# Optimization experiments

Hardware: AMD Instinct MI355X
Metric: run time of the kernel (lower is better)

## Reference

```python
import jax, jax.numpy as jnp
import numpy as np

N_P, N_A, D, H, E = 200000, 100000, 64, 32, 1000000


def setup_inputs() -> dict:
    key = jax.random.key(0)
    ks = jax.random.split(key, 32)
    inp = {}
    inp["x_paper"] = jax.random.normal(ks[0], (N_P, D), jnp.float32)
    inp["x_author"] = jax.random.normal(ks[1], (N_A, D), jnp.float32)
    inp["cites_src"] = jax.random.randint(ks[2], (E,), 0, N_P, jnp.int32)
    inp["cites_dst"] = jax.random.randint(ks[3], (E,), 0, N_P, jnp.int32)
    inp["writes_src"] = jax.random.randint(ks[4], (E,), 0, N_A, jnp.int32)
    inp["writes_dst"] = jax.random.randint(ks[5], (E,), 0, N_P, jnp.int32)
    inp["rev_src"] = jax.random.randint(ks[6], (E,), 0, N_P, jnp.int32)
    inp["rev_dst"] = jax.random.randint(ks[7], (E,), 0, N_A, jnp.int32)
    # per-relation SAGEConv params; layer 1: D->H, layer 2: H->H
    i = 8
    for layer, din in ((1, D), (2, H)):
        for rel in ("cites", "writes", "rev"):
            inp[f"W{layer}l_{rel}"] = 0.1 * jax.random.normal(ks[i], (din, H), jnp.float32); i += 1
            inp[f"W{layer}r_{rel}"] = 0.1 * jax.random.normal(ks[i], (din, H), jnp.float32); i += 1
            inp[f"b{layer}_{rel}"] = 0.01 * jax.random.normal(ks[i], (H,), jnp.float32); i += 1
    return inp


def _sage(x_src, x_dst, src, dst, Wl, Wr, b, n_dst):
    # PyG SAGEConv (aggr='mean'): lin_l(mean of source msgs) + lin_r(x_dst) + bias
    msg = x_src[src]                                              # [E, d] gather
    s = jax.ops.segment_sum(msg, dst, num_segments=n_dst)         # [n_dst, d]
    cnt = jax.ops.segment_sum(jnp.ones((src.shape[0],), x_src.dtype), dst, num_segments=n_dst)
    mean = s / jnp.maximum(cnt, 1.0)[:, None]
    return mean @ Wl + x_dst @ Wr + b


def reference(x_paper, x_author, cites_src, cites_dst, writes_src, writes_dst,
              rev_src, rev_dst,
              W1l_cites, W1r_cites, b1_cites, W1l_writes, W1r_writes, b1_writes,
              W1l_rev, W1r_rev, b1_rev,
              W2l_cites, W2r_cites, b2_cites, W2l_writes, W2r_writes, b2_writes,
              W2l_rev, W2r_rev, b2_rev):
    n_p, n_a = x_paper.shape[0], x_author.shape[0]
    # layer 1 (to_hetero sums relation outputs per dst node type), then relu
    p1 = jax.nn.relu(
        _sage(x_paper, x_paper, cites_src, cites_dst, W1l_cites, W1r_cites, b1_cites, n_p)
        + _sage(x_author, x_paper, writes_src, writes_dst, W1l_writes, W1r_writes, b1_writes, n_p))
    a1 = jax.nn.relu(
        _sage(x_paper, x_author, rev_src, rev_dst, W1l_rev, W1r_rev, b1_rev, n_a))
    # layer 2, return 'paper' output (no activation)
    p2 = (_sage(p1, p1, cites_src, cites_dst, W2l_cites, W2r_cites, b2_cites, n_p)
          + _sage(a1, p1, writes_src, writes_dst, W2l_writes, W2r_writes, b2_writes, n_p))
    return p2
```

## Files before the change

### kernel.cpp

```cpp
#include <hip/hip_runtime.h>

typedef unsigned short u16;
typedef unsigned int   u32;
typedef __attribute__((ext_vector_type(8))) short bf16x8;
typedef __attribute__((ext_vector_type(4))) float f32x4;

#define N_P 200000
#define N_A 100000
#define DD  64
#define HH  32
#define NE  1000000
#define NBP 782
#define NBA 391
#define NB4K 245
#define NCB 196
#define P4CAP 8192
#define NB_P16 12500
#define NB_A16 6250

__device__ inline float bf2f(u16 u) { return __uint_as_float(((u32)u) << 16); }
__device__ inline u16 f2bf(float f) {
    u32 u = __float_as_uint(f);
    u += 0x7fffu + ((u >> 16) & 1u);
    return (u16)(u >> 16);
}
__device__ inline float lo_f(u32 m) { return __uint_as_float(m << 16); }
__device__ inline float hi_f(u32 m) { return __uint_as_float(m & 0xffff0000u); }

__device__ inline void gseg_dual(
    const u16* __restrict__ yA, const int* __restrict__ bkA, int s0, int e0,
    const u16* __restrict__ yB, const int* __restrict__ bkB, int s1, int e1,
    int lane, float& axo, float& ayo, float& bxo, float& byo) {
    float ax = 0.f, ay = 0.f, bx = 0.f, by = 0.f;
    int lastA = min(max(e0 - 1, s0), NE - 1);
    int lastB = min(max(e1 - 1, s1), NE - 1);
    for (int j0 = s0, j1 = s1; (j0 < e0) || (j1 < e1); j0 += 8, j1 += 8) {
        int ia[8], ib[8];
#pragma unroll
        for (int i = 0; i < 8; ++i) ia[i] = bkA[min(j0 + i, lastA)];
#pragma unroll
        for (int i = 0; i < 8; ++i) ib[i] = bkB[min(j1 + i, lastB)];
        u32 ma[8], mb[8];
#pragma unroll
        for (int i = 0; i < 8; ++i)
            ma[i] = *(const u32*)(yA + (size_t)(u32)ia[i] + lane * 2);
#pragma unroll
        for (int i = 0; i < 8; ++i)
            mb[i] = *(const u32*)(yB + (size_t)(u32)ib[i] + lane * 2);
#pragma unroll
        for (int i = 0; i < 8; ++i) {
            u32 va = (j0 + i < e0) ? ma[i] : 0u;
            ax += lo_f(va); ay += hi_f(va);
        }
#pragma unroll
        for (int i = 0; i < 8; ++i) {
            u32 vb = (j1 + i < e1) ? mb[i] : 0u;
            bx += lo_f(vb); by += hi_f(vb);
        }
    }
    axo = ax; ayo = ay; bxo = bx; byo = by;
}

__global__ __launch_bounds__(256) void p1_hist_k(
    const int* __restrict__ cd, const int* __restrict__ wd, const int* __restrict__ rd,
    int* __restrict__ gsizes) {
    int rel = blockIdx.y;
    const int* dst; int shift;
    if (rel == 0)      { dst = cd; shift = 10; }
    else if (rel == 1) { dst = wd; shift = 10; }
    else               { dst = rd; shift = 9;  }
    __shared__ int cnt[256];
    int t = threadIdx.x;
    cnt[t] = 0;
    __syncthreads();
    int e0 = blockIdx.x * 4096;
#pragma unroll
    for (int i = 0; i < 16; ++i) {
        int e = e0 + i * 256 + t;
        if (e < NE) atomicAdd(&cnt[dst[e] >> shift], 1);
    }
    __syncthreads();
    if (t < NCB && cnt[t]) atomicAdd(&gsizes[rel * NCB + t], cnt[t]);
}

__global__ __launch_bounds__(256) void p2_scan_k(
    const int* __restrict__ gsizes, int* __restrict__ bases, int* __restrict__ gcur) {
    __shared__ int lds[256];
    int t = threadIdx.x;
    for (int rel = 0; rel < 3; ++rel) {
        int v = (t < NCB) ? gsizes[rel * NCB + t] : 0;
        lds[t] = v; __syncthreads();
#pragma unroll
        for (int o = 1; o < 256; o <<= 1) {
            int x = (t >= o) ? lds[t - o] : 0;
            __syncthreads();
            lds[t] += x;
            __syncthreads();
        }
        int ex = lds[t] - v;
        if (t < NCB) { bases[rel * NCB + t] = ex; gcur[rel * NCB + t] = ex; }
        __syncthreads();
    }
}

__global__ __launch_bounds__(256) void p3_bin_k(
    const int* __restrict__ cs, const int* __restrict__ cd,
    const int* __restrict__ ws_, const int* __restrict__ wd,
    const int* __restrict__ rs, const int* __restrict__ rd,
    int* __restrict__ gcur,
    u32* __restrict__ pr_c, u32* __restrict__ pr_w, u32* __restrict__ pr_r) {
    int rel = blockIdx.y;
    const int *src, *dst; int shift; u32* out;
    if (rel == 0)      { src = cs;  dst = cd; shift = 10; out = pr_c; }
    else if (rel == 1) { src = ws_; dst = wd; shift = 10; out = pr_w; }
    else               { src = rs;  dst = rd; shift = 9;  out = pr_r; }
    __shared__ u32 sbuf[4096];
    __shared__ int cnt[256], sc[256], lcur[256], gbase[256];
    int t = threadIdx.x;
    cnt[t] = 0;
    __syncthreads();
    int e0 = blockIdx.x * 4096;
    int myd[16];
#pragma unroll
    for (int i = 0; i < 16; ++i) {
        int e = e0 + i * 256 + t;
        myd[i] = (e < NE) ? dst[e] : -1;
        if (myd[i] >= 0) atomicAdd(&cnt[myd[i] >> shift], 1);
    }
    __syncthreads();
    int v = cnt[t];
    sc[t] = v; __syncthreads();
#pragma unroll
    for (int o = 1; o < 256; o <<= 1) {
        int x = (t >= o) ? sc[t - o] : 0;
        __syncthreads();
        sc[t] += x;
        __syncthreads();
    }
    int ex = sc[t] - v;
    __syncthreads();
    sc[t] = ex;
    lcur[t] = ex;
    if (t < NCB) gbase[t] = atomicAdd(&gcur[rel * NCB + t], cnt[t]);
    __syncthreads();
#pragma unroll
    for (int i = 0; i < 16; ++i) {
        int e = e0 + i * 256 + t;
        if (myd[i] >= 0) {
            int d = myd[i];
            int cb = d >> shift;
            u32 dloc = (u32)(d - (cb << shift));
            u32 pk = (dloc << 18) | (u32)src[e];
            int p = atomicAdd(&lcur[cb], 1);
            sbuf[p] = pk;
        }
    }
    __syncthreads();
    int nvalid = min(4096, NE - e0);
    for (int i = t; i < nvalid; i += 256) {
        int lo = 0, hi = NCB - 1;
        while (lo < hi) {
            int mid = (lo + hi + 1) >> 1;
            if (sc[mid] <= i) lo = mid; else hi = mid - 1;
        }
        out[gbase[lo] + (i - sc[lo])] = sbuf[i];
    }
}

__global__ __launch_bounds__(256) void p4_sort_k(
    const int* __restrict__ bases, const int* __restrict__ gsizes,
    const u32* __restrict__ pr_c, const u32* __restrict__ pr_w, const u32* __restrict__ pr_r,
    int* __restrict__ bkt_c, int* __restrict__ bkt_w, int* __restrict__ bkt_r,
    int* __restrict__ st_c, int* __restrict__ st_w, int* __restrict__ st_r) {
    int rel = blockIdx.y;
    const u32* pr; int* bkt; int* st; int width, n;
    if (rel == 0)      { pr = pr_c; bkt = bkt_c; st = st_c; width = 1024; n = N_P; }
    else if (rel == 1) { pr = pr_w; bkt = bkt_w; st = st_w; width = 1024; n = N_P; }
    else               { pr = pr_r; bkt = bkt_r; st = st_r; width = 512;  n = N_A; }
    __shared__ u32 sin[P4CAP];
    __shared__ int cnt[1024], sc2[1024], tmp[256];
    int t = threadIdx.x;
    int b = blockIdx.x;
    int base = bases[rel * NCB + b];
    int size = min(gsizes[rel * NCB + b], P4CAP);
    int d0 = b * width;
    int nd = min(width, n - d0);
    if (nd <= 0) return;
#pragma unroll
    for (int j = t; j < 1024; j += 256) cnt[j] = 0;
    __syncthreads();
    for (int i = t; i < size; i += 256) {
        u32 pk = pr[base + i];
        sin[i] = pk;
        atomicAdd(&cnt[pk >> 18], 1);
    }
    __syncthreads();
    int j0 = 4 * t;
    int c0 = cnt[j0], c1 = cnt[j0 + 1], c2 = cnt[j0 + 2], c3 = cnt[j0 + 3];
    int tot = c0 + c1 + c2 + c3;
    tmp[t] = tot; __syncthreads();
#pragma unroll
    for (int o = 1; o < 256; o <<= 1) {
        int x = (t >= o) ? tmp[t - o] : 0;
        __syncthreads();
        tmp[t] += x;
        __syncthreads();
    }
    int pre = tmp[t] - tot;
    sc2[j0] = pre;
    sc2[j0 + 1] = pre + c0;
    sc2[j0 + 2] = pre + c0 + c1;
    sc2[j0 + 3] = pre + c0 + c1 + c2;
    __syncthreads();
    for (int j = t; j < nd; j += 256) st[d0 + j] = base + sc2[j];
#pragma unroll
    for (int j = t; j < 1024; j += 256) cnt[j] = 0;
    __syncthreads();
    for (int i = t; i < size; i += 256) {
        u32 pk = sin[i];
        int dl = (int)(pk >> 18);
        int pos = sc2[dl] + atomicAdd(&cnt[dl], 1);
        bkt[base + pos] = (int)((pk & 0x3FFFFu) * HH);
    }
}

__global__ __launch_bounds__(256) void prep_w_k(
    const float* __restrict__ W1lc, const float* __restrict__ W1lr,
    const float* __restrict__ W1rc, const float* __restrict__ W1rw,
    const float* __restrict__ W1lw, const float* __restrict__ W1rr,
    const float* __restrict__ W2lc, const float* __restrict__ W2rc,
    const float* __restrict__ W2rw, const float* __restrict__ W2lw,
    const float* __restrict__ b1c, const float* __restrict__ b1w,
    const float* __restrict__ b2c, const float* __restrict__ b2w,
    u16* __restrict__ wt1h, u16* __restrict__ wt1l,
    u16* __restrict__ wt2h, u16* __restrict__ wt2l,
    float* __restrict__ b1s, float* __restrict__ b2s) {
    int m = blockIdx.x, t = threadIdx.x;
    if (m < 5) {
        const float *A = nullptr, *B = nullptr;
        if (m == 0) A = W1lc;
        else if (m == 1) A = W1lr;
        else if (m == 2) { A = W1rc; B = W1rw; }
        else if (m == 3) A = W1lw;
        else A = W1rr;
        for (int e = t; e < 2048; e += 256) {
            int k = e >> 5, n = e & 31;
            float v = A[e] + (B ? B[e] : 0.f);
            u16 h = f2bf(v);
            u16 lw = f2bf(v - bf2f(h));
            wt1h[m * 2048 + n * 64 + k] = h;
            wt1l[m * 2048 + n * 64 + k] = lw;
        }
        if (m == 2 && t < HH) b1s[t] = b1c[t] + b1w[t];
    } else {
        int mm = m - 5;
        const float *A = nullptr, *B = nullptr;
        if (mm == 0) A = W2lc;
        else if (mm == 1) { A = W2rc; B = W2rw; }
        else A = W2lw;
        for (int e = t; e < 1024; e += 256) {
            int k = e >> 5, n = e & 31;
            float v = A[e] + (B ? B[e] : 0.f);
            u16 h = f2bf(v);
            u16 lw = f2bf(v - bf2f(h));
            wt2h[mm * 1024 + n * 32 + k] = h;
            wt2l[mm * 1024 + n * 32 + k] = lw;
        }
        if (mm == 1 && t < HH) b2s[t] = b2c[t] + b2w[t];
    }
}

__global__ __launch_bounds__(256) void t1_k(
    const float* __restrict__ xp, const float* __restrict__ xa,
    const u16* __restrict__ wt1h, const u16* __restrict__ wt1l,
    const float* __restrict__ b1s, const float* __restrict__ b1r,
    u16* __restrict__ y_pc, u16* __restrict__ y_pr, u16* __restrict__ y_aw,
    u16* __restrict__ hb_p, u16* __restrict__ hb_a) {
    __shared__ float Cs[256 * 34];
    int t = threadIdx.x, w = t >> 6, l = t & 63;
    int lm = l & 15, lk = l >> 4;
    bool paper = blockIdx.x < NBP;
    int row0 = (paper ? blockIdx.x : blockIdx.x - NBP) * 256;
    const float* x = paper ? xp : xa;
    int NROW = paper ? N_P : N_A;
    int nv = min(256, NROW - row0);
    bf16x8 xh[4][2], xl[4][2];
#pragma unroll
    for (int i = 0; i < 4; ++i) {
        int rowg = min(row0 + (w * 4 + i) * 16 + lm, NROW - 1);
        const float* rp = x + (size_t)rowg * DD + lk * 8;
#pragma unroll
        for (int kc = 0; kc < 2; ++kc) {
            float4 a = *(const float4*)(rp + kc * 32);
            float4 b = *(const float4*)(rp + kc * 32 + 4);
            float f[8] = {a.x, a.y, a.z, a.w, b.x, b.y, b.z, b.w};
            union { u32 u[4]; bf16x8 v; } H, L;
#pragma unroll
            for (int j = 0; j < 4; ++j) {
                u16 h0 = f2bf(f[2 * j]), h1 = f2bf(f[2 * j + 1]);
                float l0 = f[2 * j] - bf2f(h0), l1 = f[2 * j + 1] - bf2f(h1);
                H.u[j] = (u32)h0 | ((u32)h1 << 16);
                L.u[j] = (u32)f2bf(l0) | ((u32)f2bf(l1) << 16);
            }
            xh[i][kc] = H.v; xl[i][kc] = L.v;
        }
    }
    int nw = paper ? 3 : 2;
#pragma unroll 1
    for (int iw = 0; iw < nw; ++iw) {
        int mat = paper ? iw : (3 + iw);
        const u16* Wh = wt1h + mat * 2048;
        const u16* Wl = wt1l + mat * 2048;
        bf16x8 Bh[2][2], Bl[2][2];
#pragma unroll
        for (int ct = 0; ct < 2; ++ct)
#pragma unroll
            for (int kc = 0; kc < 2; ++kc) {
                int off = (ct * 16 + lm) * 64 + kc * 32 + lk * 8;
                Bh[ct][kc] = *(const bf16x8*)(Wh + off);
                Bl[ct][kc] = *(const bf16x8*)(Wl + off);
            }
        float bv[2] = {0.f, 0.f};
        if (paper && iw == 2)  { bv[0] = b1s[lm]; bv[1] = b1s[16 + lm]; }
        if (!paper && iw == 1) { bv[0] = b1r[lm]; bv[1] = b1r[16 + lm]; }
#pragma unroll
        for (int i = 0; i < 4; ++i) {
#pragma unroll
            for (int ct = 0; ct < 2; ++ct) {
                f32x4 acc = {bv[ct], bv[ct], bv[ct], bv[ct]};
                acc = __builtin_amdgcn_mfma_f32_16x16x32_bf16(xh[i][0], Bh[ct][0], acc, 0, 0, 0);
                acc = __builtin_amdgcn_mfma_f32_16x16x32_bf16(xh[i][1], Bh[ct][1], acc, 0, 0, 0);
                acc = __builtin_amdgcn_mfma_f32_16x16x32_bf16(xl[i][0], Bh[ct][0], acc, 0, 0, 0);
                acc = __builtin_amdgcn_mfma_f32_16x16x32_bf16(xl[i][1], Bh[ct][1], acc, 0, 0, 0);
                acc = __builtin_amdgcn_mfma_f32_16x16x32_bf16(xh[i][0], Bl[ct][0], acc, 0, 0, 0);
                acc = __builtin_amdgcn_mfma_f32_16x16x32_bf16(xh[i][1], Bl[ct][1], acc, 0, 0, 0);
                int rbase = (w * 4 + i) * 16 + lk * 4;
#pragma unroll
                for (int r = 0; r < 4; ++r)
                    Cs[(rbase + r) * 34 + ct * 16 + lm] = acc[r];
            }
        }
        __syncthreads();
        u16* outp;
        if (paper) outp = (iw == 0) ? y_pc : (iw == 1) ? y_pr : hb_p;
        else       outp = (iw == 0) ? y_aw : hb_a;
        u32* g = (u32*)(outp + (size_t)row0 * HH);
#pragma unroll
        for (int p = 0; p < 4; ++p) {
            int idx = p * 256 + t;
            int row = idx >> 2, co = (idx & 3) * 8;
            if (row < nv) {
                const float* q = Cs + row * 34 + co;
                u32 o[4];
#pragma unroll
                for (int j = 0; j < 4; ++j)
                    o[j] = (u32)f2bf(q[2 * j]) | ((u32)f2bf(q[2 * j + 1]) << 16);
                *(uint4*)(g + (size_t)idx * 4) = make_uint4(o[0], o[1], o[2], o[3]);
            }
        }
        __syncthreads();
    }
}

__global__ __launch_bounds__(256) void agg1_k(
    const u16* __restrict__ y_pc, const u16* __restrict__ y_aw,
    const u16* __restrict__ y_pr,
    const int* __restrict__ st_c, const int* __restrict__ bkt_c,
    const int* __restrict__ st_w, const int* __restrict__ bkt_w,
    const int* __restrict__ st_r, const int* __restrict__ bkt_r,
    u32* __restrict__ hb_p, u32* __restrict__ hb_a) {
    int t = threadIdx.x, g = t >> 4, lane = t & 15;
    if (blockIdx.x < NB_P16) {
        int row = blockIdx.x * 16 + g;
        int s0 = st_c[row];
        int e0 = (row == N_P - 1) ? NE : st_c[row + 1];
        int s1 = st_w[row];
        int e1 = (row == N_P - 1) ? NE : st_w[row + 1];
        float cx, cy, wx, wy;
        gseg_dual(y_pc, bkt_c, s0, e0, y_aw, bkt_w, s1, e1, lane, cx, cy, wx, wy);
        int d0 = e0 - s0, d1 = e1 - s1;
        float iv0 = 1.0f / (float)(d0 < 1 ? 1 : d0);
        float iv1 = 1.0f / (float)(d1 < 1 ? 1 : d1);
        u32 self = hb_p[(size_t)row * (HH / 2) + lane];
        float ax = cx * iv0 + wx * iv1 + lo_f(self);
        float ay = cy * iv0 + wy * iv1 + hi_f(self);
        hb_p[(size_t)row * (HH / 2) + lane] = (u32)f2bf(ax) | ((u32)f2bf(ay) << 16);
    } else {
        int row = (blockIdx.x - NB_P16) * 16 + g;
        int s = st_r[row];
        int e = (row == N_A - 1) ? NE : st_r[row + 1];
        int mid = (s + e) >> 1;
        float ax0, ay0, ax1, ay1;
        gseg_dual(y_pr, bkt_r, s, mid, y_pr, bkt_r, mid, e, lane, ax0, ay0, ax1, ay1);
        int dg = e - s;
        float iv = 1.0f / (float)(dg < 1 ? 1 : dg);
        u32 self = hb_a[(size_t)row * (HH / 2) + lane];
        float ax = (ax0 + ax1) * iv + lo_f(self);
        float ay = (ay0 + ay1) * iv + hi_f(self);
        hb_a[(size_t)row * (HH / 2) + lane] = (u32)f2bf(ax) | ((u32)f2bf(ay) << 16);
    }
}

__global__ __launch_bounds__(256) void t2_k(
    const u32* __restrict__ hb_p, const u32* __restrict__ hb_a,
    const u16* __restrict__ wt2h, const u16* __restrict__ wt2l,
    const float* __restrict__ b2s,
    u16* __restrict__ z_p, u16* __restrict__ z_a, float* __restrict__ hp2) {
    __shared__ float Cs[256 * 34];
    int t = threadIdx.x, w = t >> 6, l = t & 63;
    int lm = l & 15, lk = l >> 4;
    bool paper = blockIdx.x < NBP;
    int row0 = (paper ? blockIdx.x : blockIdx.x - NBP) * 256;
    const u32* hb = paper ? hb_p : hb_a;
    int NROW = paper ? N_P : N_A;
    int nv = min(256, NROW - row0);
    bf16x8 af[4];
#pragma unroll
    for (int i = 0; i < 4; ++i) {
        int rowg = min(row0 + (w * 4 + i) * 16 + lm, NROW - 1);
        uint4 q = *(const uint4*)(hb + (size_t)rowg * (HH / 2) + lk * 4);
        u32 qq[4] = {q.x, q.y, q.z, q.w};
        union { u32 u[4]; bf16x8 v; } A;
#pragma unroll
        for (int j = 0; j < 4; ++j) {
            u32 m = ((qq[j] & 0x80008000u) >> 15) * 0xFFFFu;
            A.u[j] = qq[j] & ~m;
        }
        af[i] = A.v;
    }
    int nw = paper ? 2 : 1;
#pragma unroll 1
    for (int iw = 0; iw < nw; ++iw) {
        int mat = paper ? iw : 2;
        const u16* Wh = wt2h + mat * 1024;
        const u16* Wl = wt2l + mat * 1024;
        bf16x8 Bh[2], Bl[2];
#pragma unroll
        for (int ct = 0; ct < 2; ++ct) {
            int off = (ct * 16 + lm) * 32 + lk * 8;
            Bh[ct] = *(const bf16x8*)(Wh + off);
            Bl[ct] = *(const bf16x8*)(Wl + off);
        }
        float bv[2] = {0.f, 0.f};
        if (paper && iw == 1) { bv[0] = b2s[lm]; bv[1] = b2s[16 + lm]; }
#pragma unroll
        for (int i = 0; i < 4; ++i) {
#pragma unroll
            for (int ct = 0; ct < 2; ++ct) {
                f32x4 acc = {bv[ct], bv[ct], bv[ct], bv[ct]};
                acc = __builtin_amdgcn_mfma_f32_16x16x32_bf16(af[i], Bh[ct], acc, 0, 0, 0);
                acc = __builtin_amdgcn_mfma_f32_16x16x32_bf16(af[i], Bl[ct], acc, 0, 0, 0);
                int rbase = (w * 4 + i) * 16 + lk * 4;
#pragma unroll
                for (int r = 0; r < 4; ++r)
                    Cs[(rbase + r) * 34 + ct * 16 + lm] = acc[r];
            }
        }
        __syncthreads();
        if (paper && iw == 1) {
            float* g = hp2 + (size_t)row0 * HH;
#pragma unroll
            for (int p = 0; p < 8; ++p) {
                int idx = p * 256 + t;
                int row = idx >> 3, co = (idx & 7) * 4;
                if (row < nv) {
                    const float* q = Cs + row * 34 + co;
                    *(float4*)(g + (size_t)row * HH + co) = make_float4(q[0], q[1], q[2], q[3]);
                }
            }
        } else {
            u16* outp = paper ? z_p : z_a;
            u32* g = (u32*)(outp + (size_t)row0 * HH);
#pragma unroll
            for (int p = 0; p < 4; ++p) {
                int idx = p * 256 + t;
                int row = idx >> 2, co = (idx & 3) * 8;
                if (row < nv) {
                    const float* q = Cs + row * 34 + co;
                    u32 o[4];
#pragma unroll
                    for (int j = 0; j < 4; ++j)
                        o[j] = (u32)f2bf(q[2 * j]) | ((u32)f2bf(q[2 * j + 1]) << 16);
                    *(uint4*)(g + (size_t)idx * 4) = make_uint4(o[0], o[1], o[2], o[3]);
                }
            }
        }
        __syncthreads();
    }
}

__global__ __launch_bounds__(256) void agg2_k(
    const u16* __restrict__ z_p, const u16* __restrict__ z_a,
    const int* __restrict__ st_c, const int* __restrict__ bkt_c,
    const int* __restrict__ st_w, const int* __restrict__ bkt_w,
    const float* __restrict__ hp2, float* __restrict__ out) {
    int t = threadIdx.x, g = t >> 4, lane = t & 15;
    int row = blockIdx.x * 16 + g;
    int s0 = st_c[row];
    int e0 = (row == N_P - 1) ? NE : st_c[row + 1];
    int s1 = st_w[row];
    int e1 = (row == N_P - 1) ? NE : st_w[row + 1];
    float cx, cy, wx, wy;
    gseg_dual(z_p, bkt_c, s0, e0, z_a, bkt_w, s1, e1, lane, cx, cy, wx, wy);
    int d0 = e0 - s0, d1 = e1 - s1;
    float iv0 = 1.0f / (float)(d0 < 1 ? 1 : d0);
    float iv1 = 1.0f / (float)(d1 < 1 ? 1 : d1);
    float2 h = *(const float2*)(hp2 + (size_t)row * HH + lane * 2);
    float2 o = make_float2(h.x + cx * iv0 + wx * iv1,
                           h.y + cy * iv0 + wy * iv1);
    *(float2*)(out + (size_t)row * HH + lane * 2) = o;
}

extern "C" void kernel_launch(void* const* d_in, const int* in_sizes, int n_in,
                              void* d_out, int out_size, void* d_ws, size_t ws_size,
                              hipStream_t stream) {
    const float* x_p  = (const float*)d_in[0];
    const float* x_a  = (const float*)d_in[1];
    const int* c_src  = (const int*)d_in[2];
    const int* c_dst  = (const int*)d_in[3];
    const int* w_src  = (const int*)d_in[4];
    const int* w_dst  = (const int*)d_in[5];
    const int* r_src  = (const int*)d_in[6];
    const int* r_dst  = (const int*)d_in[7];
    const float* W1l_c = (const float*)d_in[8];
    const float* W1r_c = (const float*)d_in[9];
    const float* b1_c  = (const float*)d_in[10];
    const float* W1l_w = (const float*)d_in[11];
    const float* W1r_w = (const float*)d_in[12];
    const float* b1_w  = (const float*)d_in[13];
    const float* W1l_r = (const float*)d_in[14];
    const float* W1r_r = (const float*)d_in[15];
    const float* b1_r  = (const float*)d_in[16];
    const float* W2l_c = (const float*)d_in[17];
    const float* W2r_c = (const float*)d_in[18];
    const float* b2_c  = (const float*)d_in[19];
    const float* W2l_w = (const float*)d_in[20];
    const float* W2r_w = (const float*)d_in[21];
    const float* b2_w  = (const float*)d_in[22];

    int* gsizes = (int*)d_ws;
    int* bases  = gsizes + 3 * NCB;
    int* gcur   = bases + 3 * NCB;
    int* st_c   = gcur + 3 * NCB;
    int* st_w   = st_c + N_P;
    int* st_r   = st_w + N_P;
    int* bkt_c  = st_r + N_A;
    int* bkt_w  = bkt_c + NE;
    int* bkt_r  = bkt_w + NE;
    u16* wt1h  = (u16*)(bkt_r + NE);
    u16* wt1l  = wt1h + 5 * 2048;
    u16* wt2h  = wt1l + 5 * 2048;
    u16* wt2l  = wt2h + 3 * 1024;
    float* b1s = (float*)(wt2l + 3 * 1024);
    float* b2s = b1s + HH;
    u16* hb_p  = (u16*)(b2s + HH);
    u16* hb_a  = hb_p + (size_t)N_P * HH;
    u16* y_pc  = hb_a + (size_t)N_A * HH;
    u16* y_pr  = y_pc + (size_t)N_P * HH;
    u16* y_aw  = y_pr + (size_t)N_P * HH;
    float* hp2 = (float*)(y_aw + (size_t)N_A * HH);
    u32* pr_c  = (u32*)hp2;
    u32* pr_w  = pr_c + NE;
    u32* pr_r  = pr_w + NE;
    u16* z_p   = y_pc;
    u16* z_a   = y_aw;
    float* outp = (float*)d_out;

    const size_t need = ((uintptr_t)(hp2 + (size_t)N_P * HH)) - (uintptr_t)d_ws;
    if (ws_size < need) return;

    hipMemsetAsync(gsizes, 0, 3 * NCB * sizeof(int), stream);
    prep_w_k<<<8, 256, 0, stream>>>(W1l_c, W1l_r, W1r_c, W1r_w, W1l_w, W1r_r,
                                    W2l_c, W2r_c, W2r_w, W2l_w,
                                    b1_c, b1_w, b2_c, b2_w,
                                    wt1h, wt1l, wt2h, wt2l, b1s, b2s);
    p1_hist_k<<<dim3(NB4K, 3), 256, 0, stream>>>(c_dst, w_dst, r_dst, gsizes);
    p2_scan_k<<<1, 256, 0, stream>>>(gsizes, bases, gcur);
    p3_bin_k<<<dim3(NB4K, 3), 256, 0, stream>>>(c_src, c_dst, w_src, w_dst, r_src, r_dst,
                                                gcur, pr_c, pr_w, pr_r);
    p4_sort_k<<<dim3(NCB, 3), 256, 0, stream>>>(bases, gsizes, pr_c, pr_w, pr_r,
                                                bkt_c, bkt_w, bkt_r, st_c, st_w, st_r);
    t1_k<<<NBP + NBA, 256, 0, stream>>>(x_p, x_a, wt1h, wt1l, b1s, b1_r,
                                        y_pc, y_pr, y_aw, hb_p, hb_a);
    agg1_k<<<NB_P16 + NB_A16, 256, 0, stream>>>(y_pc, y_aw, y_pr,
                                                st_c, bkt_c, st_w, bkt_w, st_r, bkt_r,
                                                (u32*)hb_p, (u32*)hb_a);
    t2_k<<<NBP + NBA, 256, 0, stream>>>((const u32*)hb_p, (const u32*)hb_a,
                                        wt2h, wt2l, b2s, z_p, z_a, hp2);
    agg2_k<<<NB_P16, 256, 0, stream>>>(z_p, z_a, st_c, bkt_c, st_w, bkt_w, hp2, outp);
}
```

Baseline: 406.4 us.

## Vectorize edge loads in binning, fold memset into prep, drop block syncs in GEMMs

The histogram and binning kernels now read dst/src with int4 vector loads, and binning keeps src values in registers instead of re-reading them from global memory. The gsizes memset is replaced by zeroing inside prep_w_k, which removes one launch. In t1_k and t2_k each wave now writes back only its own 64 rows from LDS, so the block-wide __syncthreads are replaced by an LDS waitcnt and a compiler barrier. The within-block edge order in binning changes (each thread now owns 4 consecutive edges), and the per-wave writeback relies on each wave touching only its own slice of Cs.

```diff
diff --git a/kernel.cpp b/kernel.cpp
--- a/kernel.cpp
+++ b/kernel.cpp
@@ -74,10 +74,22 @@
     cnt[t] = 0;
     __syncthreads();
     int e0 = blockIdx.x * 4096;
-#pragma unroll
-    for (int i = 0; i < 16; ++i) {
-        int e = e0 + i * 256 + t;
-        if (e < NE) atomicAdd(&cnt[dst[e] >> shift], 1);
+    if (e0 + 4096 <= NE) {
+        const int4* dv = (const int4*)(dst + e0);
+#pragma unroll
+        for (int i = 0; i < 4; ++i) {
+            int4 v = dv[i * 256 + t];
+            atomicAdd(&cnt[v.x >> shift], 1);
+            atomicAdd(&cnt[v.y >> shift], 1);
+            atomicAdd(&cnt[v.z >> shift], 1);
+            atomicAdd(&cnt[v.w >> shift], 1);
+        }
+    } else {
+#pragma unroll
+        for (int i = 0; i < 16; ++i) {
+            int e = e0 + i * 256 + t;
+            if (e < NE) atomicAdd(&cnt[dst[e] >> shift], 1);
+        }
     }
     __syncthreads();
     if (t < NCB && cnt[t]) atomicAdd(&gsizes[rel * NCB + t], cnt[t]);
@@ -120,12 +132,34 @@
     cnt[t] = 0;
     __syncthreads();
     int e0 = blockIdx.x * 4096;
-    int myd[16];
-#pragma unroll
-    for (int i = 0; i < 16; ++i) {
-        int e = e0 + i * 256 + t;
-        myd[i] = (e < NE) ? dst[e] : -1;
-        if (myd[i] >= 0) atomicAdd(&cnt[myd[i] >> shift], 1);
+    int myd[16], mys[16];
+    if (e0 + 4096 <= NE) {
+        const int4* dv = (const int4*)(dst + e0);
+        const int4* sv = (const int4*)(src + e0);
+#pragma unroll
+        for (int i = 0; i < 4; ++i) {
+            int4 v = dv[i * 256 + t];
+            int4 s = sv[i * 256 + t];
+            myd[4 * i] = v.x; myd[4 * i + 1] = v.y; myd[4 * i + 2] = v.z; myd[4 * i + 3] = v.w;
+            mys[4 * i] = s.x; mys[4 * i + 1] = s.y; mys[4 * i + 2] = s.z; mys[4 * i + 3] = s.w;
+            atomicAdd(&cnt[v.x >> shift], 1);
+            atomicAdd(&cnt[v.y >> shift], 1);
+            atomicAdd(&cnt[v.z >> shift], 1);
+            atomicAdd(&cnt[v.w >> shift], 1);
+        }
+    } else {
+#pragma unroll
+        for (int i = 0; i < 4; ++i) {
+#pragma unroll
+            for (int c = 0; c < 4; ++c) {
+                int e = e0 + (i * 256 + t) * 4 + c;
+                int idx = 4 * i + c;
+                if (e < NE) {
+                    myd[idx] = dst[e]; mys[idx] = src[e];
+                    atomicAdd(&cnt[myd[idx] >> shift], 1);
+                } else { myd[idx] = -1; mys[idx] = 0; }
+            }
+        }
     }
     __syncthreads();
     int v = cnt[t];
@@ -145,12 +179,11 @@
     __syncthreads();
 #pragma unroll
     for (int i = 0; i < 16; ++i) {
-        int e = e0 + i * 256 + t;
         if (myd[i] >= 0) {
             int d = myd[i];
             int cb = d >> shift;
             u32 dloc = (u32)(d - (cb << shift));
-            u32 pk = (dloc << 18) | (u32)src[e];
+            u32 pk = (dloc << 18) | (u32)mys[i];
             int p = atomicAdd(&lcur[cb], 1);
             sbuf[p] = pk;
         }
@@ -234,8 +267,12 @@
     const float* __restrict__ b2c, const float* __restrict__ b2w,
     u16* __restrict__ wt1h, u16* __restrict__ wt1l,
     u16* __restrict__ wt2h, u16* __restrict__ wt2l,
-    float* __restrict__ b1s, float* __restrict__ b2s) {
+    float* __restrict__ b1s, float* __restrict__ b2s,
+    int* __restrict__ gsizes) {
     int m = blockIdx.x, t = threadIdx.x;
+    if (m == 0) {
+        for (int e = t; e < 3 * NCB; e += 256) gsizes[e] = 0;
+    }
     if (m < 5) {
         const float *A = nullptr, *B = nullptr;
         if (m == 0) A = W1lc;
@@ -287,7 +324,7 @@
     bf16x8 xh[4][2], xl[4][2];
 #pragma unroll
     for (int i = 0; i < 4; ++i) {
-        int rowg = min(row0 + (w * 4 + i) * 16 + lm, NROW - 1);
+        int rowg = min(row0 + w * 64 + i * 16 + lm, NROW - 1);
         const float* rp = x + (size_t)rowg * DD + lk * 8;
 #pragma unroll
         for (int kc = 0; kc < 2; ++kc) {
@@ -334,31 +371,31 @@
                 acc = __builtin_amdgcn_mfma_f32_16x16x32_bf16(xl[i][1], Bh[ct][1], acc, 0, 0, 0);
                 acc = __builtin_amdgcn_mfma_f32_16x16x32_bf16(xh[i][0], Bl[ct][0], acc, 0, 0, 0);
                 acc = __builtin_amdgcn_mfma_f32_16x16x32_bf16(xh[i][1], Bl[ct][1], acc, 0, 0, 0);
-                int rbase = (w * 4 + i) * 16 + lk * 4;
+                int rbase = w * 64 + i * 16 + lk * 4;
 #pragma unroll
                 for (int r = 0; r < 4; ++r)
                     Cs[(rbase + r) * 34 + ct * 16 + lm] = acc[r];
             }
         }
-        __syncthreads();
+        asm volatile("s_waitcnt lgkmcnt(0)" ::: "memory");
         u16* outp;
         if (paper) outp = (iw == 0) ? y_pc : (iw == 1) ? y_pr : hb_p;
         else       outp = (iw == 0) ? y_aw : hb_a;
         u32* g = (u32*)(outp + (size_t)row0 * HH);
 #pragma unroll
         for (int p = 0; p < 4; ++p) {
-            int idx = p * 256 + t;
-            int row = idx >> 2, co = (idx & 3) * 8;
-            if (row < nv) {
-                const float* q = Cs + row * 34 + co;
+            int j = p * 64 + l;
+            int rl = w * 64 + (j >> 2);
+            if (rl < nv) {
+                const float* q = Cs + rl * 34 + (j & 3) * 8;
                 u32 o[4];
 #pragma unroll
-                for (int j = 0; j < 4; ++j)
-                    o[j] = (u32)f2bf(q[2 * j]) | ((u32)f2bf(q[2 * j + 1]) << 16);
-                *(uint4*)(g + (size_t)idx * 4) = make_uint4(o[0], o[1], o[2], o[3]);
-            }
-        }
-        __syncthreads();
+                for (int jj = 0; jj < 4; ++jj)
+                    o[jj] = (u32)f2bf(q[2 * jj]) | ((u32)f2bf(q[2 * jj + 1]) << 16);
+                *(uint4*)(g + ((size_t)w * 256 + j) * 4) = make_uint4(o[0], o[1], o[2], o[3]);
+            }
+        }
+        asm volatile("" ::: "memory");
     }
 }
 
@@ -417,7 +454,7 @@
     bf16x8 af[4];
 #pragma unroll
     for (int i = 0; i < 4; ++i) {
-        int rowg = min(row0 + (w * 4 + i) * 16 + lm, NROW - 1);
+        int rowg = min(row0 + w * 64 + i * 16 + lm, NROW - 1);
         uint4 q = *(const uint4*)(hb + (size_t)rowg * (HH / 2) + lk * 4);
         u32 qq[4] = {q.x, q.y, q.z, q.w};
         union { u32 u[4]; bf16x8 v; } A;
@@ -450,22 +487,23 @@
                 f32x4 acc = {bv[ct], bv[ct], bv[ct], bv[ct]};
                 acc = __builtin_amdgcn_mfma_f32_16x16x32_bf16(af[i], Bh[ct], acc, 0, 0, 0);
                 acc = __builtin_amdgcn_mfma_f32_16x16x32_bf16(af[i], Bl[ct], acc, 0, 0, 0);
-                int rbase = (w * 4 + i) * 16 + lk * 4;
+                int rbase = w * 64 + i * 16 + lk * 4;
 #pragma unroll
                 for (int r = 0; r < 4; ++r)
                     Cs[(rbase + r) * 34 + ct * 16 + lm] = acc[r];
             }
         }
-        __syncthreads();
+        asm volatile("s_waitcnt lgkmcnt(0)" ::: "memory");
         if (paper && iw == 1) {
-            float* g = hp2 + (size_t)row0 * HH;
+            float* gf = hp2 + (size_t)row0 * HH;
 #pragma unroll
             for (int p = 0; p < 8; ++p) {
-                int idx = p * 256 + t;
-                int row = idx >> 3, co = (idx & 7) * 4;
-                if (row < nv) {
-                    const float* q = Cs + row * 34 + co;
-                    *(float4*)(g + (size_t)row * HH + co) = make_float4(q[0], q[1], q[2], q[3]);
+                int j = p * 64 + l;
+                int rl = w * 64 + (j >> 3);
+                if (rl < nv) {
+                    const float* q = Cs + rl * 34 + (j & 7) * 4;
+                    *(float4*)(gf + ((size_t)w * 512 + j) * 4) =
+                        make_float4(q[0], q[1], q[2], q[3]);
                 }
             }
         } else {
@@ -473,19 +511,19 @@
             u32* g = (u32*)(outp + (size_t)row0 * HH);
 #pragma unroll
             for (int p = 0; p < 4; ++p) {
-                int idx = p * 256 + t;
-                int row = idx >> 2, co = (idx & 3) * 8;
-                if (row < nv) {
-                    const float* q = Cs + row * 34 + co;
+                int j = p * 64 + l;
+                int rl = w * 64 + (j >> 2);
+                if (rl < nv) {
+                    const float* q = Cs + rl * 34 + (j & 3) * 8;
                     u32 o[4];
 #pragma unroll
-                    for (int j = 0; j < 4; ++j)
-                        o[j] = (u32)f2bf(q[2 * j]) | ((u32)f2bf(q[2 * j + 1]) << 16);
-                    *(uint4*)(g + (size_t)idx * 4) = make_uint4(o[0], o[1], o[2], o[3]);
+                    for (int jj = 0; jj < 4; ++jj)
+                        o[jj] = (u32)f2bf(q[2 * jj]) | ((u32)f2bf(q[2 * jj + 1]) << 16);
+                    *(uint4*)(g + ((size_t)w * 256 + j) * 4) = make_uint4(o[0], o[1], o[2], o[3]);
                 }
             }
         }
-        __syncthreads();
+        asm volatile("" ::: "memory");
     }
 }
 
@@ -569,11 +607,10 @@
     const size_t need = ((uintptr_t)(hp2 + (size_t)N_P * HH)) - (uintptr_t)d_ws;
     if (ws_size < need) return;
 
-    hipMemsetAsync(gsizes, 0, 3 * NCB * sizeof(int), stream);
     prep_w_k<<<8, 256, 0, stream>>>(W1l_c, W1l_r, W1r_c, W1r_w, W1l_w, W1r_r,
                                     W2l_c, W2r_c, W2r_w, W2l_w,
                                     b1_c, b1_w, b2_c, b2_w,
-                                    wt1h, wt1l, wt2h, wt2l, b1s, b2s);
+                                    wt1h, wt1l, wt2h, wt2l, b1s, b2s, gsizes);
     p1_hist_k<<<dim3(NB4K, 3), 256, 0, stream>>>(c_dst, w_dst, r_dst, gsizes);
     p2_scan_k<<<1, 256, 0, stream>>>(gsizes, bases, gcur);
     p3_bin_k<<<dim3(NB4K, 3), 256, 0, stream>>>(c_src, c_dst, w_src, w_dst, r_src, r_dst,
```

After: 395.3 us. 1.03x faster.
